# Kernel tuning notes

Hardware: AMD Instinct MI355X
Metric: run time of the kernel (lower is better)

The kernel has to match this reference:

```python
import jax, jax.numpy as jnp
import numpy as np

K = 56          # kernel_size (attended axis length)
HEADS = 8
IN_C = 64
OUT_C = 64
DH = OUT_C // HEADS  # 8; q,k use DH//2=4 channels, v uses DH=8
F_QR = 0.1
F_KR = 0.1
F_SVE = 0.1
F_SV = 1.0
EPS = 1e-5


def _bn(x, g, b, axes):
    # batch-norm in training mode: batch statistics over `axes`, affine per channel dim 1
    m = jnp.mean(x, axes, keepdims=True)
    v = jnp.var(x, axes, keepdims=True)
    shp = [1] * x.ndim
    shp[1] = -1
    return (x - m) * jax.lax.rsqrt(v + EPS) * g.reshape(shp) + b.reshape(shp)


def setup_inputs() -> dict:
    key = jax.random.key(0)
    ks = jax.random.split(key, 3)
    x = jax.random.normal(ks[0], (1, IN_C, 32, 56, K), dtype=jnp.float32)
    w_qkv = jax.random.normal(ks[1], (2 * OUT_C, IN_C), dtype=jnp.float32) * np.sqrt(1.0 / IN_C)
    relative = jax.random.normal(ks[2], (2 * DH, 2 * K - 1), dtype=jnp.float32) * np.sqrt(1.0 / DH)
    return {
        "x": x,
        "w_qkv": w_qkv,
        "relative": relative,
        "bn_qkv_g": jnp.ones((2 * OUT_C,), jnp.float32),
        "bn_qkv_b": jnp.zeros((2 * OUT_C,), jnp.float32),
        "bn_sim_g": jnp.ones((3 * HEADS,), jnp.float32),
        "bn_sim_b": jnp.zeros((3 * HEADS,), jnp.float32),
        "bn_out_g": jnp.ones((2 * OUT_C,), jnp.float32),
        "bn_out_b": jnp.zeros((2 * OUT_C,), jnp.float32),
    }


def reference(x, w_qkv, relative, bn_qkv_g, bn_qkv_b, bn_sim_g, bn_sim_b, bn_out_g, bn_out_b):
    N, C, D, Hdim, Wdim = x.shape  # axial='width': attend over W == K
    xp = jnp.transpose(x, (0, 2, 3, 1, 4)).reshape(N * D * Hdim, C, Wdim)  # (B, C, K)
    # 1x1 conv1d (no bias) + BN1d
    qkv = jnp.einsum("bci,oc->boi", xp, w_qkv)
    qkv = _bn(qkv, bn_qkv_g, bn_qkv_b, (0, 2))
    qkv = qkv.reshape(-1, HEADS, 2 * DH, K)
    q = qkv[:, :, : DH // 2]
    k = qkv[:, :, DH // 2 : DH]
    v = qkv[:, :, DH:]
    # relative position embeddings: emb[c,i,j] = relative[c, i - j + K - 1]
    idx = jnp.arange(K)
    rel_idx = idx[:, None] - idx[None, :] + K - 1  # (K, K)
    emb = relative[:, rel_idx]  # (2*DH, K, K)
    q_e, k_e, v_e = emb[: DH // 2], emb[DH // 2 : DH], emb[DH:]
    qr = jnp.einsum("bgci,cij->bgij", q, q_e) * F_QR
    kr = jnp.transpose(jnp.einsum("bgci,cij->bgij", k, k_e), (0, 1, 3, 2)) * F_KR
    qk = jnp.einsum("bgci,bgcj->bgij", q, k)
    stacked = jnp.concatenate([qk, qr, kr], axis=1)  # (B, 3*heads, K, K)
    stacked = _bn(stacked, bn_sim_g, bn_sim_b, (0, 2, 3))
    sim = jax.nn.softmax(stacked.reshape(-1, 3, HEADS, K, K).sum(axis=1), axis=3)
    sv = jnp.einsum("bgij,bgcj->bgci", sim, v) * F_SV
    sve = jnp.einsum("bgij,cij->bgci", sim, v_e) * F_SVE
    so = jnp.concatenate([sv, sve], axis=-1).reshape(-1, 2 * OUT_C, K)
    so = _bn(so, bn_out_g, bn_out_b, (0, 2))
    out = so.reshape(N, D, Hdim, OUT_C, 2, K).sum(axis=4)
    return jnp.transpose(out, (0, 3, 1, 2, 4))  # back to (N, OUT_C, D, H, W)
```

## Files before the change

### kernel.cpp

```cpp
#include <hip/hip_runtime.h>
#include <math.h>

typedef float v2f __attribute__((ext_vector_type(2)));

constexpr int KW      = 56;
constexpr int NB      = 1792;
constexpr int QKV_CH  = 128;
constexpr int SIM_CH  = 24;
constexpr int SLOTS   = 64;
constexpr int SMASK   = 63;
constexpr float EPS   = 1e-5f;

constexpr int   PA[10]  = {0,0,0,0,1,1,1,2,2,3};
constexpr int   PB[10]  = {0,1,2,3,1,2,3,2,3,3};
constexpr float PMf[10] = {1,2,2,2,1,2,2,1,2,1};

#if __has_builtin(__builtin_amdgcn_exp2f)
#define EXP2(x) __builtin_amdgcn_exp2f(x)
#else
#define EXP2(x) __expf((x) * 0.6931471805599453f)
#endif

#define HTREE_STEP(M, HALF)                                         \
    {                                                               \
        const bool up_ = (lane & (M)) != 0;                         \
        _Pragma("unroll")                                           \
        for (int v = 0; v < (HALF); ++v) {                          \
            float a_ = up_ ? red[v + (HALF)] : red[v];              \
            float s_ = up_ ? red[v] : red[v + (HALF)];              \
            red[v] = a_ + __shfl_xor(s_, (M));                      \
        }                                                           \
    }

__global__ __launch_bounds__(256) void k_qkv(const float* __restrict__ x,
                                             const float* __restrict__ w,
                                             const float* __restrict__ rel,
                                             float* __restrict__ qkv,
                                             float* __restrict__ sums,
                                             float* __restrict__ tabs) {
    const int t = threadIdx.x;
    if (blockIdx.x >= NB) {
        const int t0 = (blockIdx.x - NB) * 256 + t;
        const int STR = 8 * 256;
        float* Rq  = tabs;
        float* Rk  = tabs + 224;
        float* E2q = tabs + 448;
        float* E2k = tabs + 1008;
        float4* TQF = (float4*)(tabs + 1568);
        float4* TVF = (float4*)(tabs + 2464);
        for (int idx = t0; idx < 448; idx += STR) {
            int which = idx / 224, r = idx % 224;
            int i = r >> 2, c = r & 3;
            const float* src = rel + (which * 4 + c) * 111;
            float s = 0.f;
            for (int tt = 0; tt < 56; ++tt) s += src[i + tt];
            (which ? Rk : Rq)[r] = s;
        }
        for (int idx = t0; idx < 1120; idx += STR) {
            int which = idx / 560, r = idx % 560;
            int i = r / 10, p = r % 10;
            const float* sa = rel + (which * 4 + PA[p]) * 111;
            const float* sb = rel + (which * 4 + PB[p]) * 111;
            float s = 0.f;
            for (int tt = 0; tt < 56; ++tt) s += sa[i + tt] * sb[i + tt];
            (which ? E2k : E2q)[r] = s;
        }
        for (int d = t0; d < 112; d += STR) {
            bool v = d < 111;
            float4 tq, tk, ta, tb;
            tq.x = v ? rel[0 * 111 + d] : 0.f;
            tq.y = v ? rel[1 * 111 + d] : 0.f;
            tq.z = v ? rel[2 * 111 + d] : 0.f;
            tq.w = v ? rel[3 * 111 + d] : 0.f;
            tk.x = v ? rel[4 * 111 + 110 - d] : 0.f;
            tk.y = v ? rel[5 * 111 + 110 - d] : 0.f;
            tk.z = v ? rel[6 * 111 + 110 - d] : 0.f;
            tk.w = v ? rel[7 * 111 + 110 - d] : 0.f;
            ta.x = v ? rel[8 * 111 + d] : 0.f;
            ta.y = v ? rel[9 * 111 + d] : 0.f;
            ta.z = v ? rel[10 * 111 + d] : 0.f;
            ta.w = v ? rel[11 * 111 + d] : 0.f;
            tb.x = v ? rel[12 * 111 + d] : 0.f;
            tb.y = v ? rel[13 * 111 + d] : 0.f;
            tb.z = v ? rel[14 * 111 + d] : 0.f;
            tb.w = v ? rel[15 * 111 + d] : 0.f;
            TQF[d]       = tq;
            TQF[112 + d] = tk;
            TVF[d]       = ta;
            TVF[112 + d] = tb;
        }
        return;
    }
    __shared__ float xs[64 * KW];
    __shared__ float wt[64 * 132];
    __shared__ float s1[128], s2[128];
    const int b = blockIdx.x;

    if (t < 128) { s1[t] = 0.f; s2[t] = 0.f; }
    for (int idx = t; idx < 896; idx += 256) {
        int c = idx / 14, r = idx % 14;
        float4 v = *(const float4*)&x[c * 100352 + b * 56 + r * 4];
        *(float4*)&xs[c * 56 + r * 4] = v;
    }
    for (int idx = t; idx < 2048; idx += 256) {
        int o = idx >> 4, cq = idx & 15;
        float4 v = *(const float4*)&w[o * 64 + cq * 4];
        wt[(cq * 4 + 0) * 132 + o] = v.x;
        wt[(cq * 4 + 1) * 132 + o] = v.y;
        wt[(cq * 4 + 2) * 132 + o] = v.z;
        wt[(cq * 4 + 3) * 132 + o] = v.w;
    }
    __syncthreads();

    if (t < 224) {
        const int ob = t & 31, ib = t >> 5;
        v2f acc[4][4];
#pragma unroll
        for (int o = 0; o < 4; ++o)
#pragma unroll
            for (int ip = 0; ip < 4; ++ip) acc[o][ip] = (v2f)(0.f);
        for (int c = 0; c < 64; ++c) {
            float4 wv = *(const float4*)&wt[c * 132 + (ob << 2)];
            float4 x0 = *(const float4*)&xs[c * 56 + (ib << 3)];
            float4 x1 = *(const float4*)&xs[c * 56 + (ib << 3) + 4];
            v2f xp[4];
            xp[0] = (v2f){x0.x, x0.y}; xp[1] = (v2f){x0.z, x0.w};
            xp[2] = (v2f){x1.x, x1.y}; xp[3] = (v2f){x1.z, x1.w};
            v2f wd[4];
            wd[0] = (v2f)(wv.x); wd[1] = (v2f)(wv.y);
            wd[2] = (v2f)(wv.z); wd[3] = (v2f)(wv.w);
#pragma unroll
            for (int o = 0; o < 4; ++o)
#pragma unroll
                for (int ip = 0; ip < 4; ++ip)
                    acc[o][ip] += wd[o] * xp[ip];
        }
#pragma unroll
        for (int i = 0; i < 8; ++i) {
            float4 st;
            st.x = acc[0][i >> 1][i & 1];
            st.y = acc[1][i >> 1][i & 1];
            st.z = acc[2][i >> 1][i & 1];
            st.w = acc[3][i >> 1][i & 1];
            *(float4*)&qkv[b * 7168 + (ib * 8 + i) * 128 + ob * 4] = st;
        }
#pragma unroll
        for (int o = 0; o < 4; ++o) {
            float ps = 0.f, ps2 = 0.f;
#pragma unroll
            for (int ip = 0; ip < 4; ++ip) {
                ps  += acc[o][ip].x + acc[o][ip].y;
                ps2 += acc[o][ip].x * acc[o][ip].x + acc[o][ip].y * acc[o][ip].y;
            }
            atomicAdd(&s1[ob * 4 + o], ps);
            atomicAdd(&s2[ob * 4 + o], ps2);
        }
    }
    __syncthreads();
    if (t < 128) {
        float* dst = sums + (b & SMASK) * 256;
        atomicAdd(&dst[t], s1[t]);
        atomicAdd(&dst[128 + t], s2[t]);
    }
}

__global__ void k_coef(const float* __restrict__ sums, const float* __restrict__ g,
                       const float* __restrict__ bb, float* __restrict__ coef,
                       int nch, float invM) {
    const int o = blockIdx.x;
    const int s = threadIdx.x;
    float a1 = sums[s * 2 * nch + o];
    float a2 = sums[s * 2 * nch + nch + o];
#pragma unroll
    for (int mk = 1; mk < 64; mk <<= 1) {
        a1 += __shfl_xor(a1, mk);
        a2 += __shfl_xor(a2, mk);
    }
    if (s == 0) {
        float mean = a1 * invM;
        float var  = fmaxf(a2 * invM - mean * mean, 0.f);
        float sc   = g[o] * rsqrtf(var + EPS);
        coef[o] = sc;
        coef[nch + o] = bb[o] - mean * sc;
    }
}

__global__ __launch_bounds__(256) void k_simstats(const float* __restrict__ qkv,
                                                  const float* __restrict__ qcoef,
                                                  const float* __restrict__ Rq,
                                                  const float* __restrict__ Rk,
                                                  const float* __restrict__ E2q,
                                                  const float* __restrict__ E2k,
                                                  float* __restrict__ ssum) {
    __shared__ float Sst[4][32];
    const int wid = threadIdx.x >> 6, lane = threadIdx.x & 63;
    const int unit = blockIdx.x * 4 + wid;
    const int b = unit >> 3, g = unit & 7;
    const int iL = lane < 56 ? lane : 55;
    const float valid = lane < 56 ? 1.f : 0.f;

    const float* row = qkv + b * 7168 + iL * 128 + g * 16;
    float4 q4 = *(const float4*)(row);
    float4 k4 = *(const float4*)(row + 4);
    const float4 aq = *(const float4*)&qcoef[g * 16];
    const float4 ak = *(const float4*)&qcoef[g * 16 + 4];
    const float4 cq = *(const float4*)&qcoef[QKV_CH + g * 16];
    const float4 ck = *(const float4*)&qcoef[QKV_CH + g * 16 + 4];
    float qv[4], kv[4];
    qv[0] = (q4.x * aq.x + cq.x) * valid;
    qv[1] = (q4.y * aq.y + cq.y) * valid;
    qv[2] = (q4.z * aq.z + cq.z) * valid;
    qv[3] = (q4.w * aq.w + cq.w) * valid;
    kv[0] = (k4.x * ak.x + ck.x) * valid;
    kv[1] = (k4.y * ak.y + ck.y) * valid;
    kv[2] = (k4.z * ak.z + ck.z) * valid;
    kv[3] = (k4.w * ak.w + ck.w) * valid;

    float4 rq = *(const float4*)&Rq[iL * 4];
    float4 rk = *(const float4*)&Rk[iL * 4];
    float e2q[10], e2k[10];
#pragma unroll
    for (int p = 0; p < 10; ++p) { e2q[p] = E2q[iL * 10 + p]; e2k[p] = E2k[iL * 10 + p]; }

    float red[32];
#pragma unroll
    for (int c = 0; c < 4; ++c) { red[c] = qv[c]; red[4 + c] = kv[c]; }
#pragma unroll
    for (int p = 0; p < 10; ++p) {
        red[8 + p]  = qv[PA[p]] * qv[PB[p]];
        red[18 + p] = kv[PA[p]] * kv[PB[p]];
    }
    {
        float rqa[4] = {rq.x, rq.y, rq.z, rq.w};
        float rka[4] = {rk.x, rk.y, rk.z, rk.w};
        float pq = 0.f, pk = 0.f, pq2 = 0.f, pk2_ = 0.f;
#pragma unroll
        for (int c = 0; c < 4; ++c) { pq += qv[c] * rqa[c]; pk += kv[c] * rka[c]; }
#pragma unroll
        for (int p = 0; p < 10; ++p) {
            pq2 += PMf[p] * red[8 + p]  * e2q[p];
            pk2_ += PMf[p] * red[18 + p] * e2k[p];
        }
        red[28] = pq; red[29] = pk; red[30] = pq2; red[31] = pk2_;
    }
    HTREE_STEP(1, 16)
    HTREE_STEP(2, 8)
    HTREE_STEP(4, 4)
    HTREE_STEP(8, 2)
    HTREE_STEP(16, 1)
    red[0] += __shfl_xor(red[0], 32);
    const int vIdx = ((lane & 1) << 4) | ((lane & 2) << 2) | (lane & 4)
                   | ((lane & 8) >> 2) | ((lane & 16) >> 4);
    if (lane < 32) Sst[wid][vIdx] = red[0];
    __syncthreads();
    if (lane == 0) {
        float S[32];
#pragma unroll
        for (int q = 0; q < 8; ++q) {
            float4 f = *(const float4*)&Sst[wid][q * 4];
            S[q * 4] = f.x; S[q * 4 + 1] = f.y; S[q * 4 + 2] = f.z; S[q * 4 + 3] = f.w;
        }
        float sqk = S[0] * S[4] + S[1] * S[5] + S[2] * S[6] + S[3] * S[7];
        float sqk2 = 0.f;
#pragma unroll
        for (int p = 0; p < 10; ++p) sqk2 += PMf[p] * S[8 + p] * S[18 + p];
        float* ss = ssum + (blockIdx.x & SMASK) * 48;
        atomicAdd(&ss[g], sqk);
        atomicAdd(&ss[8 + g], 0.1f * S[28]);
        atomicAdd(&ss[16 + g], 0.1f * S[29]);
        atomicAdd(&ss[SIM_CH + g], sqk2);
        atomicAdd(&ss[SIM_CH + 8 + g], 0.01f * S[30]);
        atomicAdd(&ss[SIM_CH + 16 + g], 0.01f * S[31]);
    }
}

__global__ __launch_bounds__(256) void k_attn(const float* __restrict__ qkv,
                                              const float* __restrict__ qcoef,
                                              const float* __restrict__ scoef,
                                              const float4* __restrict__ TQF,
                                              const float4* __restrict__ TVF,
                                              float* __restrict__ sv2,
                                              float* __restrict__ sve2,
                                              float* __restrict__ osums) {
    __shared__ float4 TQs[224];
    __shared__ float4 TVs[224];
    __shared__ float4 KVs[4 * 168];
    const int t = threadIdx.x;
    const int wid = t >> 6, lane = t & 63;
    const int unit = blockIdx.x * 4 + wid;
    const int b = unit >> 3, g = unit & 7;
    const int iL = lane < 56 ? lane : 55;

    if (t < 224) { TQs[t] = TQF[t]; TVs[t] = TVF[t]; }

    const float* row = qkv + b * 7168 + iL * 128 + g * 16;
    float4 q4  = *(const float4*)(row);
    float4 k4  = *(const float4*)(row + 4);
    float4 va4 = *(const float4*)(row + 8);
    float4 vb4 = *(const float4*)(row + 12);
    const float4 a0 = *(const float4*)&qcoef[g * 16];
    const float4 a1 = *(const float4*)&qcoef[g * 16 + 4];
    const float4 a2 = *(const float4*)&qcoef[g * 16 + 8];
    const float4 a3 = *(const float4*)&qcoef[g * 16 + 12];
    const float4 c0 = *(const float4*)&qcoef[QKV_CH + g * 16];
    const float4 c1 = *(const float4*)&qcoef[QKV_CH + g * 16 + 4];
    const float4 c2 = *(const float4*)&qcoef[QKV_CH + g * 16 + 8];
    const float4 c3 = *(const float4*)&qcoef[QKV_CH + g * 16 + 12];
    float4 kh, vh, wh;
    kh.x = k4.x * a1.x + c1.x;  kh.y = k4.y * a1.y + c1.y;
    kh.z = k4.z * a1.z + c1.z;  kh.w = k4.w * a1.w + c1.w;
    vh.x = va4.x * a2.x + c2.x; vh.y = va4.y * a2.y + c2.y;
    vh.z = va4.z * a2.z + c2.z; vh.w = va4.w * a2.w + c2.w;
    wh.x = vb4.x * a3.x + c3.x; wh.y = vb4.y * a3.y + c3.y;
    wh.z = vb4.z * a3.z + c3.z; wh.w = vb4.w * a3.w + c3.w;
    float qh[4];
    qh[0] = q4.x * a0.x + c0.x;  qh[1] = q4.y * a0.y + c0.y;
    qh[2] = q4.z * a0.z + c0.z;  qh[3] = q4.w * a0.w + c0.w;

    KVs[wid * 168 + iL]       = kh;
    KVs[wid * 168 + 56 + iL]  = vh;
    KVs[wid * 168 + 112 + iL] = wh;
    __syncthreads();

    const float L2E = 1.44269504088896340736f;
    const float aqk = scoef[g] * L2E;
    const float aqr = scoef[8 + g] * 0.1f * L2E;
    const float akr = scoef[16 + g] * 0.1f * L2E;
    const float cc2 = (scoef[SIM_CH + g] + scoef[SIM_CH + 8 + g]
                       + scoef[SIM_CH + 16 + g]) * L2E;
    const v2f qa01 = {qh[0] * aqk, qh[1] * aqk};
    const v2f qa23 = {qh[2] * aqk, qh[3] * aqk};
    const v2f qr01 = {qh[0] * aqr, qh[1] * aqr};
    const v2f qr23 = {qh[2] * aqr, qh[3] * aqr};
    const v2f akrp = {akr, akr};

    float l = 0.f;
    v2f sva = (v2f)(0.f), svb = (v2f)(0.f), svc = (v2f)(0.f), svd = (v2f)(0.f);
    v2f sea = (v2f)(0.f), seb = (v2f)(0.f), sec = (v2f)(0.f), sed = (v2f)(0.f);

    const float4* tqp = TQs + 55 + iL;
    const float4* tvp = TVs + 55 + iL;
    const float4* kvp = KVs + wid * 168;

#pragma unroll 4
    for (int j = 0; j < 56; ++j) {
        float4 tq = tqp[-j];
        float4 tk = tqp[112 - j];
        float4 ta = tvp[-j];
        float4 tb = tvp[112 - j];
        float4 kj = kvp[j];
        float4 vj = kvp[56 + j];
        float4 wj = kvp[112 + j];
        v2f u01 = akrp * (v2f){tk.x, tk.y} + qa01;
        v2f u23 = akrp * (v2f){tk.z, tk.w} + qa23;
        v2f acc = u01 * (v2f){kj.x, kj.y};
        acc += u23 * (v2f){kj.z, kj.w};
        acc += qr01 * (v2f){tq.x, tq.y};
        acc += qr23 * (v2f){tq.z, tq.w};
        float e = EXP2(acc.x + acc.y + cc2);
        l += e;
        v2f ep = {e, e};
        sva += ep * (v2f){vj.x, vj.y};
        svb += ep * (v2f){vj.z, vj.w};
        svc += ep * (v2f){wj.x, wj.y};
        svd += ep * (v2f){wj.z, wj.w};
        sea += ep * (v2f){ta.x, ta.y};
        seb += ep * (v2f){ta.z, ta.w};
        sec += ep * (v2f){tb.x, tb.y};
        sed += ep * (v2f){tb.z, tb.w};
    }
    const float inv = 1.f / l;
    const float inv1 = 0.1f * inv;
    float osv[8], ose[8];
    osv[0] = sva.x * inv;  osv[1] = sva.y * inv;
    osv[2] = svb.x * inv;  osv[3] = svb.y * inv;
    osv[4] = svc.x * inv;  osv[5] = svc.y * inv;
    osv[6] = svd.x * inv;  osv[7] = svd.y * inv;
    ose[0] = sea.x * inv1; ose[1] = sea.y * inv1;
    ose[2] = seb.x * inv1; ose[3] = seb.y * inv1;
    ose[4] = sec.x * inv1; ose[5] = sec.y * inv1;
    ose[6] = sed.x * inv1; ose[7] = sed.y * inv1;

    if (lane < 56) {
        size_t base = ((size_t)(g * 8) * 1792 + b) * 56 + iL;
#pragma unroll
        for (int c = 0; c < 8; ++c) {
            sv2[base + (size_t)c * 100352]  = osv[c];
            sve2[base + (size_t)c * 100352] = ose[c];
        }
    }
    const float valid = lane < 56 ? 1.f : 0.f;
    float red[32];
#pragma unroll
    for (int c = 0; c < 8; ++c) {
        red[c]      = osv[c] * valid;
        red[8 + c]  = ose[c] * valid;
        red[16 + c] = osv[c] * osv[c] * valid;
        red[24 + c] = ose[c] * ose[c] * valid;
    }
    HTREE_STEP(1, 16)
    HTREE_STEP(2, 8)
    HTREE_STEP(4, 4)
    HTREE_STEP(8, 2)
    HTREE_STEP(16, 1)
    red[0] += __shfl_xor(red[0], 32);
    if (lane < 32) {
        const int v = ((lane & 1) << 4) | ((lane & 2) << 2) | (lane & 4)
                    | ((lane & 8) >> 2) | ((lane & 16) >> 4);
        const int addr = ((v >> 4) & 1) * 128 + g * 16 + 2 * (v & 7) + ((v >> 3) & 1);
        float* dst = osums + (blockIdx.x & SMASK) * 256;
        atomicAdd(&dst[addr], red[0]);
    }
}

__global__ __launch_bounds__(256) void k_out(const float* __restrict__ sv2,
                                             const float* __restrict__ sve2,
                                             const float* __restrict__ ocoef,
                                             float* __restrict__ out) {
    int e4 = blockIdx.x * 256 + threadIdx.x;
    int i0 = e4 * 4;
    int oc = i0 / 100352;
    int o0 = 2 * oc;
    float A = ocoef[o0], B = ocoef[o0 + 1];
    float C = ocoef[QKV_CH + o0] + ocoef[QKV_CH + o0 + 1];
    float4 v0 = *(const float4*)&sv2[i0];
    float4 v1 = *(const float4*)&sve2[i0];
    float4 r;
    r.x = A * v0.x + B * v1.x + C;
    r.y = A * v0.y + B * v1.y + C;
    r.z = A * v0.z + B * v1.z + C;
    r.w = A * v0.w + B * v1.w + C;
    *(float4*)&out[i0] = r;
}

extern "C" void kernel_launch(void* const* d_in, const int* in_sizes, int n_in,
                              void* d_out, int out_size, void* d_ws, size_t ws_size,
                              hipStream_t stream) {
    const float* x     = (const float*)d_in[0];
    const float* wqkv  = (const float*)d_in[1];
    const float* rel   = (const float*)d_in[2];
    const float* g_qkv = (const float*)d_in[3];
    const float* b_qkv = (const float*)d_in[4];
    const float* g_sim = (const float*)d_in[5];
    const float* b_sim = (const float*)d_in[6];
    const float* g_out = (const float*)d_in[7];
    const float* b_out = (const float*)d_in[8];
    float* out = (float*)d_out;
    float* ws = (float*)d_ws;

    float* qkv_raw  = ws;
    float* sv2      = ws + 12845056;
    float* sve2     = ws + 19267584;
    float* stats    = ws + 25690112;
    float* sums_buf = stats;
    float* qkv_coef = stats + 16384;
    float* sim_coef = stats + 16640;
    float* out_coef = stats + 16688;
    float* tabs     = stats + 16944;
    float* Rq   = tabs;
    float* Rk   = tabs + 224;
    float* E2q  = tabs + 448;
    float* E2k  = tabs + 1008;
    float4* TQF = (float4*)(tabs + 1568);
    float4* TVF = (float4*)(tabs + 2464);

    hipMemsetAsync(sums_buf, 0, SLOTS * 256 * sizeof(float), stream);

    k_qkv<<<NB + 8, 256, 0, stream>>>(x, wqkv, rel, qkv_raw, sums_buf, tabs);
    k_coef<<<QKV_CH, 64, 0, stream>>>(sums_buf, g_qkv, b_qkv, qkv_coef, QKV_CH,
                                      1.0f / 100352.0f);
    hipMemsetAsync(sums_buf, 0, SLOTS * 48 * sizeof(float), stream);
    k_simstats<<<3584, 256, 0, stream>>>(qkv_raw, qkv_coef, Rq, Rk, E2q, E2k,
                                         sums_buf);
    k_coef<<<SIM_CH, 64, 0, stream>>>(sums_buf, g_sim, b_sim, sim_coef, SIM_CH,
                                      1.0f / 5619712.0f);
    hipMemsetAsync(sums_buf, 0, SLOTS * 256 * sizeof(float), stream);
    k_attn<<<3584, 256, 0, stream>>>(qkv_raw, qkv_coef, sim_coef, TQF, TVF,
                                     sv2, sve2, sums_buf);
    k_coef<<<QKV_CH, 64, 0, stream>>>(sums_buf, g_out, b_out, out_coef, QKV_CH,
                                      1.0f / 100352.0f);
    k_out<<<6272, 256, 0, stream>>>(sv2, sve2, out_coef, out);
}
```

Before: 230.4 us.

## Pack attention outputs and value-embedding table as bf16 and merge stat memsets

Result: faster. 216.3 us (-6.1%).

```diff
diff --git a/kernel.cpp b/kernel.cpp
--- a/kernel.cpp
+++ b/kernel.cpp
@@ -20,6 +20,16 @@
 #else
 #define EXP2(x) __expf((x) * 0.6931471805599453f)
 #endif
+
+__device__ inline unsigned bfr(float f) {
+    unsigned u = __float_as_uint(f);
+    return (u + 0x7fffu + ((u >> 16) & 1u)) >> 16;
+}
+__device__ inline unsigned pk2(float a, float b) {
+    return bfr(a) | (bfr(b) << 16);
+}
+__device__ inline float blo(unsigned u) { return __uint_as_float(u << 16); }
+__device__ inline float bhi(unsigned u) { return __uint_as_float(u & 0xffff0000u); }
 
 #define HTREE_STEP(M, HALF)                                         \
     {                                                               \
@@ -47,7 +57,7 @@
         float* E2q = tabs + 448;
         float* E2k = tabs + 1008;
         float4* TQF = (float4*)(tabs + 1568);
-        float4* TVF = (float4*)(tabs + 2464);
+        uint4*  TVB = (uint4*)(tabs + 2464);
         for (int idx = t0; idx < 448; idx += STR) {
             int which = idx / 224, r = idx % 224;
             int i = r >> 2, c = r & 3;
@@ -86,8 +96,8 @@
             tb.w = v ? rel[15 * 111 + d] : 0.f;
             TQF[d]       = tq;
             TQF[112 + d] = tk;
-            TVF[d]       = ta;
-            TVF[112 + d] = tb;
+            TVB[d] = make_uint4(pk2(ta.x, ta.y), pk2(ta.z, ta.w),
+                                pk2(tb.x, tb.y), pk2(tb.z, tb.w));
         }
         return;
     }
@@ -278,12 +288,11 @@
                                               const float* __restrict__ qcoef,
                                               const float* __restrict__ scoef,
                                               const float4* __restrict__ TQF,
-                                              const float4* __restrict__ TVF,
-                                              float* __restrict__ sv2,
-                                              float* __restrict__ sve2,
+                                              const uint4* __restrict__ TVB,
+                                              unsigned* __restrict__ svp,
                                               float* __restrict__ osums) {
     __shared__ float4 TQs[224];
-    __shared__ float4 TVs[224];
+    __shared__ uint4  Tvb[112];
     __shared__ float4 KVs[4 * 168];
     const int t = threadIdx.x;
     const int wid = t >> 6, lane = t & 63;
@@ -291,7 +300,8 @@
     const int b = unit >> 3, g = unit & 7;
     const int iL = lane < 56 ? lane : 55;
 
-    if (t < 224) { TQs[t] = TQF[t]; TVs[t] = TVF[t]; }
+    if (t < 224) TQs[t] = TQF[t];
+    if (t < 112) Tvb[t] = TVB[t];
 
     const float* row = qkv + b * 7168 + iL * 128 + g * 16;
     float4 q4  = *(const float4*)(row);
@@ -336,18 +346,18 @@
 
     float l = 0.f;
     v2f sva = (v2f)(0.f), svb = (v2f)(0.f), svc = (v2f)(0.f), svd = (v2f)(0.f);
-    v2f sea = (v2f)(0.f), seb = (v2f)(0.f), sec = (v2f)(0.f), sed = (v2f)(0.f);
+    float se0 = 0.f, se1 = 0.f, se2 = 0.f, se3 = 0.f;
+    float se4 = 0.f, se5 = 0.f, se6 = 0.f, se7 = 0.f;
 
     const float4* tqp = TQs + 55 + iL;
-    const float4* tvp = TVs + 55 + iL;
+    const uint4*  Bp  = Tvb + 55 + iL;
     const float4* kvp = KVs + wid * 168;
 
 #pragma unroll 4
     for (int j = 0; j < 56; ++j) {
         float4 tq = tqp[-j];
         float4 tk = tqp[112 - j];
-        float4 ta = tvp[-j];
-        float4 tb = tvp[112 - j];
+        uint4  B  = Bp[-j];
         float4 kj = kvp[j];
         float4 vj = kvp[56 + j];
         float4 wj = kvp[112 + j];
@@ -364,10 +374,10 @@
         svb += ep * (v2f){vj.z, vj.w};
         svc += ep * (v2f){wj.x, wj.y};
         svd += ep * (v2f){wj.z, wj.w};
-        sea += ep * (v2f){ta.x, ta.y};
-        seb += ep * (v2f){ta.z, ta.w};
-        sec += ep * (v2f){tb.x, tb.y};
-        sed += ep * (v2f){tb.z, tb.w};
+        se0 += e * blo(B.x); se1 += e * bhi(B.x);
+        se2 += e * blo(B.y); se3 += e * bhi(B.y);
+        se4 += e * blo(B.z); se5 += e * bhi(B.z);
+        se6 += e * blo(B.w); se7 += e * bhi(B.w);
     }
     const float inv = 1.f / l;
     const float inv1 = 0.1f * inv;
@@ -376,18 +386,16 @@
     osv[2] = svb.x * inv;  osv[3] = svb.y * inv;
     osv[4] = svc.x * inv;  osv[5] = svc.y * inv;
     osv[6] = svd.x * inv;  osv[7] = svd.y * inv;
-    ose[0] = sea.x * inv1; ose[1] = sea.y * inv1;
-    ose[2] = seb.x * inv1; ose[3] = seb.y * inv1;
-    ose[4] = sec.x * inv1; ose[5] = sec.y * inv1;
-    ose[6] = sed.x * inv1; ose[7] = sed.y * inv1;
+    ose[0] = se0 * inv1; ose[1] = se1 * inv1;
+    ose[2] = se2 * inv1; ose[3] = se3 * inv1;
+    ose[4] = se4 * inv1; ose[5] = se5 * inv1;
+    ose[6] = se6 * inv1; ose[7] = se7 * inv1;
 
     if (lane < 56) {
         size_t base = ((size_t)(g * 8) * 1792 + b) * 56 + iL;
 #pragma unroll
-        for (int c = 0; c < 8; ++c) {
-            sv2[base + (size_t)c * 100352]  = osv[c];
-            sve2[base + (size_t)c * 100352] = ose[c];
-        }
+        for (int c = 0; c < 8; ++c)
+            svp[base + (size_t)c * 100352] = pk2(osv[c], ose[c]);
     }
     const float valid = lane < 56 ? 1.f : 0.f;
     float red[32];
@@ -413,8 +421,7 @@
     }
 }
 
-__global__ __launch_bounds__(256) void k_out(const float* __restrict__ sv2,
-                                             const float* __restrict__ sve2,
+__global__ __launch_bounds__(256) void k_out(const unsigned* __restrict__ svp,
                                              const float* __restrict__ ocoef,
                                              float* __restrict__ out) {
     int e4 = blockIdx.x * 256 + threadIdx.x;
@@ -423,13 +430,12 @@
     int o0 = 2 * oc;
     float A = ocoef[o0], B = ocoef[o0 + 1];
     float C = ocoef[QKV_CH + o0] + ocoef[QKV_CH + o0 + 1];
-    float4 v0 = *(const float4*)&sv2[i0];
-    float4 v1 = *(const float4*)&sve2[i0];
+    uint4 p = *(const uint4*)&svp[i0];
     float4 r;
-    r.x = A * v0.x + B * v1.x + C;
-    r.y = A * v0.y + B * v1.y + C;
-    r.z = A * v0.z + B * v1.z + C;
-    r.w = A * v0.w + B * v1.w + C;
+    r.x = A * blo(p.x) + B * bhi(p.x) + C;
+    r.y = A * blo(p.y) + B * bhi(p.y) + C;
+    r.z = A * blo(p.z) + B * bhi(p.z) + C;
+    r.w = A * blo(p.w) + B * bhi(p.w) + C;
     *(float4*)&out[i0] = r;
 }
 
@@ -448,36 +454,35 @@
     float* out = (float*)d_out;
     float* ws = (float*)d_ws;
 
-    float* qkv_raw  = ws;
-    float* sv2      = ws + 12845056;
-    float* sve2     = ws + 19267584;
-    float* stats    = ws + 25690112;
-    float* sums_buf = stats;
-    float* qkv_coef = stats + 16384;
-    float* sim_coef = stats + 16640;
-    float* out_coef = stats + 16688;
-    float* tabs     = stats + 16944;
+    float*    qkv_raw = ws;
+    unsigned* svp     = (unsigned*)(ws + 12845056);
+    float* stats      = ws + 25690112;
+    float* qkv_sums = stats;
+    float* sim_sums = stats + 16384;
+    float* out_sums = stats + 19456;
+    float* qkv_coef = stats + 35840;
+    float* sim_coef = stats + 36096;
+    float* out_coef = stats + 36144;
+    float* tabs     = stats + 36400;
     float* Rq   = tabs;
     float* Rk   = tabs + 224;
     float* E2q  = tabs + 448;
     float* E2k  = tabs + 1008;
     float4* TQF = (float4*)(tabs + 1568);
-    float4* TVF = (float4*)(tabs + 2464);
-
-    hipMemsetAsync(sums_buf, 0, SLOTS * 256 * sizeof(float), stream);
-
-    k_qkv<<<NB + 8, 256, 0, stream>>>(x, wqkv, rel, qkv_raw, sums_buf, tabs);
-    k_coef<<<QKV_CH, 64, 0, stream>>>(sums_buf, g_qkv, b_qkv, qkv_coef, QKV_CH,
+    uint4*  TVB = (uint4*)(tabs + 2464);
+
+    hipMemsetAsync(stats, 0, 35840 * sizeof(float), stream);
+
+    k_qkv<<<NB + 8, 256, 0, stream>>>(x, wqkv, rel, qkv_raw, qkv_sums, tabs);
+    k_coef<<<QKV_CH, 64, 0, stream>>>(qkv_sums, g_qkv, b_qkv, qkv_coef, QKV_CH,
                                       1.0f / 100352.0f);
-    hipMemsetAsync(sums_buf, 0, SLOTS * 48 * sizeof(float), stream);
     k_simstats<<<3584, 256, 0, stream>>>(qkv_raw, qkv_coef, Rq, Rk, E2q, E2k,
-                                         sums_buf);
-    k_coef<<<SIM_CH, 64, 0, stream>>>(sums_buf, g_sim, b_sim, sim_coef, SIM_CH,
+                                         sim_sums);
+    k_coef<<<SIM_CH, 64, 0, stream>>>(sim_sums, g_sim, b_sim, sim_coef, SIM_CH,
                                       1.0f / 5619712.0f);
-    hipMemsetAsync(sums_buf, 0, SLOTS * 256 * sizeof(float), stream);
-    k_attn<<<3584, 256, 0, stream>>>(qkv_raw, qkv_coef, sim_coef, TQF, TVF,
-                                     sv2, sve2, sums_buf);
-    k_coef<<<QKV_CH, 64, 0, stream>>>(sums_buf, g_out, b_out, out_coef, QKV_CH,
+    k_attn<<<3584, 256, 0, stream>>>(qkv_raw, qkv_coef, sim_coef, TQF, TVB,
+                                     svp, out_sums);
+    k_coef<<<QKV_CH, 64, 0, stream>>>(out_sums, g_out, b_out, out_coef, QKV_CH,
                                       1.0f / 100352.0f);
-    k_out<<<6272, 256, 0, stream>>>(sv2, sve2, out_coef, out);
-}
+    k_out<<<6272, 256, 0, stream>>>(svp, out_coef, out);
+}
```
